# Optimization experiments

Measured on AMD Instinct MI355X. Metric: run time of the kernel, lower is better.

Reference implementation:

```python
import jax, jax.numpy as jnp
import numpy as np

S = 4096            # num tokens (single causal sequence)
HID = 1024          # hidden_size
NH = 16             # num query heads
NKV = 4             # num kv heads
HD = 64             # head_dim
THETA = 10000.0
Q_SIZE = NH * HD
KV_SIZE = NKV * HD


def setup_inputs() -> dict:
    key = jax.random.key(0)
    k1, k2, k3 = jax.random.split(key, 3)
    return {
        "positions": jnp.arange(S, dtype=jnp.int32),
        "hidden_states": jax.random.normal(k1, (S, 2 * HID), dtype=jnp.float32),
        "w_qkv": jax.random.normal(k2, (Q_SIZE + 2 * KV_SIZE, 2 * HID), dtype=jnp.float32) * 0.02,
        "w_o": jax.random.normal(k3, (HID, Q_SIZE), dtype=jnp.float32) * 0.02,
    }


def _rope(x, positions):
    # x: [S, H, HD]; neox-style rotate-half RoPE
    half = HD // 2
    inv_freq = 1.0 / (THETA ** (jnp.arange(0, half, dtype=jnp.float32) / half))
    freqs = positions.astype(jnp.float32)[:, None] * inv_freq  # [S, half]
    cos = jnp.cos(freqs)[:, None, :]  # [S, 1, half]
    sin = jnp.sin(freqs)[:, None, :]
    x1, x2 = x[..., :half], x[..., half:]
    return jnp.concatenate([x1 * cos - x2 * sin, x2 * cos + x1 * sin], axis=-1)


def reference(positions, hidden_states, w_qkv, w_o):
    qkv = hidden_states @ w_qkv.T  # [S, Q_SIZE + 2*KV_SIZE]
    q = qkv[:, :Q_SIZE].reshape(S, NH, HD)
    k = qkv[:, Q_SIZE:Q_SIZE + KV_SIZE].reshape(S, NKV, HD)
    v = qkv[:, Q_SIZE + KV_SIZE:].reshape(S, NKV, HD)
    q = _rope(q, positions)
    k = _rope(k, positions)
    # GQA: group query heads over kv heads
    g = NH // NKV
    qg = q.reshape(S, NKV, g, HD)
    scale = HD ** -0.5
    scores = jnp.einsum("qhgd,thd->hgqt", qg, k) * scale  # [NKV, g, S, S]
    causal = positions[:, None] >= positions[None, :]      # [S, S]
    scores = jnp.where(causal[None, None], scores, jnp.finfo(scores.dtype).min)
    probs = jax.nn.softmax(scores, axis=-1)
    o = jnp.einsum("hgqt,thd->qhgd", probs, v).reshape(S, Q_SIZE)
    return o @ w_o.T  # [S, HID]
```

## Files before the change

### kernel.cpp

```cpp
#include <hip/hip_runtime.h>
#include <math.h>

#define S_LEN   4096
#define NHEADS  16
#define NKVH    4
#define HDIM    64
#define QKV_N   1536
#define HID2    2048
#define OUT_N   1024

typedef __attribute__((ext_vector_type(8))) __bf16 bf16x8;
typedef __attribute__((ext_vector_type(4))) __bf16 bf16x4;
typedef __attribute__((ext_vector_type(4))) float  f32x4;
typedef __attribute__((ext_vector_type(16))) float f32x16;
typedef __attribute__((ext_vector_type(4))) unsigned int u32x4;

#define GL_LDS16(gaddr, laddr)                                                  \
  __builtin_amdgcn_global_load_lds(                                             \
      (const __attribute__((address_space(1))) unsigned int*)(gaddr),           \
      (__attribute__((address_space(3))) unsigned int*)(laddr), 16, 0, 0)

__device__ __forceinline__ unsigned cvt_pk_bf16(float lo, float hi) {
  unsigned r;
  asm("v_cvt_pk_bf16_f32 %0, %1, %2" : "=v"(r) : "v"(lo), "v"(hi));
  return r;
}

__global__ __launch_bounds__(256) void cvt_all(const float* __restrict__ hid,
                                               const float* __restrict__ wq,
                                               const float* __restrict__ wo,
                                               __bf16* __restrict__ hid_bf,
                                               __bf16* __restrict__ wq_bf,
                                               __bf16* __restrict__ wo_bf) {
  const int n1 = S_LEN * HID2;
  const int n2 = QKV_N * HID2;
  int i = (blockIdx.x * blockDim.x + threadIdx.x) * 8;
  const float* src; __bf16* dst; int off;
  if (i < n1)           { src = hid; dst = hid_bf; off = i; }
  else if (i < n1 + n2) { src = wq;  dst = wq_bf;  off = i - n1; }
  else                  { src = wo;  dst = wo_bf;  off = i - n1 - n2; }
  float4 a = *(const float4*)(src + off);
  float4 b = *(const float4*)(src + off + 4);
  bf16x8 o = {(__bf16)a.x,(__bf16)a.y,(__bf16)a.z,(__bf16)a.w,
              (__bf16)b.x,(__bf16)b.y,(__bf16)b.z,(__bf16)b.w};
  *(bf16x8*)(dst + off) = o;
}

__global__ __launch_bounds__(256) void rope_table(const int* __restrict__ positions,
                                                  float* __restrict__ ct,
                                                  float* __restrict__ st) {
  int i = blockIdx.x * blockDim.x + threadIdx.x;
  int s = i >> 5, d = i & 31;
  double inv = pow(10000.0, -(double)d / 32.0);
  double fr = (double)positions[s] * inv;
  ct[i] = (float)cos(fr);
  st[i] = (float)sin(fr);
}

template<int BM, bool C_BF16>
__global__ __launch_bounds__(256) void gemm_db(const __bf16* __restrict__ A,
                                               const __bf16* __restrict__ B,
                                               void* __restrict__ Cp,
                                               int M, int N, int K) {
  constexpr int TM = BM / 32;
  __shared__ __align__(16) __bf16 As[2 * BM * 32];
  __shared__ __align__(16) __bf16 Bs[2 * 128 * 32];
  const int tid  = threadIdx.x;
  const int bm   = blockIdx.x, bn = blockIdx.y;
  const int wave = tid >> 6, lane = tid & 63;
  const int quad = lane >> 4, col = lane & 15;
  const int wm = (wave >> 1) * (BM / 2), wn = (wave & 1) * 64;

  const int lrow = lane >> 2, lcol = (lane & 3) * 8;
  const __bf16* Ag = A + (size_t)(bm * BM + wave * (BM / 4) + lrow) * K + lcol;
  const __bf16* Bg = B + (size_t)(bn * 128 + wave * 32 + lrow) * K + lcol;
  __bf16* AsW = As + wave * (BM / 4) * 32;
  __bf16* BsW = Bs + wave * 32 * 32;

  f32x4 acc[TM][4];
#pragma unroll
  for (int i = 0; i < TM; ++i)
#pragma unroll
    for (int j = 0; j < 4; ++j) acc[i][j] = (f32x4){0.f, 0.f, 0.f, 0.f};

#pragma unroll
  for (int u = 0; u < BM / 64; ++u)
    GL_LDS16(Ag + (size_t)(u * 16) * K, AsW + u * 16 * 32);
  GL_LDS16(Bg,                  BsW);
  GL_LDS16(Bg + (size_t)16 * K, BsW + 16 * 32);
  __syncthreads();

  int cur = 0;
  for (int kk = 0; kk < K; kk += 32) {
    if (kk + 32 < K) {
      const int nxt = cur ^ 1;
#pragma unroll
      for (int u = 0; u < BM / 64; ++u)
        GL_LDS16(Ag + kk + 32 + (size_t)(u * 16) * K,
                 AsW + nxt * BM * 32 + u * 16 * 32);
      GL_LDS16(Bg + kk + 32,                  BsW + nxt * 128 * 32);
      GL_LDS16(Bg + kk + 32 + (size_t)16 * K, BsW + nxt * 128 * 32 + 16 * 32);
    }

    bf16x8 a[TM], b[4];
#pragma unroll
    for (int tm = 0; tm < TM; ++tm)
      a[tm] = *(const bf16x8*)&As[cur * BM * 32 + (wm + tm * 16 + col) * 32 + quad * 8];
#pragma unroll
    for (int tn = 0; tn < 4; ++tn)
      b[tn] = *(const bf16x8*)&Bs[cur * 128 * 32 + (wn + tn * 16 + col) * 32 + quad * 8];
#pragma unroll
    for (int tm = 0; tm < TM; ++tm)
#pragma unroll
      for (int tn = 0; tn < 4; ++tn)
        acc[tm][tn] = __builtin_amdgcn_mfma_f32_16x16x32_bf16(a[tm], b[tn], acc[tm][tn], 0, 0, 0);

    __syncthreads();
    cur ^= 1;
  }

#pragma unroll
  for (int tm = 0; tm < TM; ++tm)
#pragma unroll
    for (int tn = 0; tn < 4; ++tn) {
      int row = bm * BM + wm + tm * 16 + quad * 4;
      int cg  = bn * 128 + wn + tn * 16 + col;
#pragma unroll
      for (int r = 0; r < 4; ++r) {
        if constexpr (C_BF16)
          ((__bf16*)Cp)[(size_t)(row + r) * N + cg] = (__bf16)acc[tm][tn][r];
        else
          ((float*)Cp)[(size_t)(row + r) * N + cg] = acc[tm][tn][r];
      }
    }
}

__global__ __launch_bounds__(256) void rope_cast(const __bf16* __restrict__ qkv,
                                                 const float* __restrict__ ct,
                                                 const float* __restrict__ st,
                                                 __bf16* __restrict__ qb,
                                                 __bf16* __restrict__ kb) {
  int g = blockIdx.x * blockDim.x + threadIdx.x;
  int d = g & 31;
  int rem = g >> 5;
  int head = rem % 20;
  int s = rem / 20;
  bool isq = head < NHEADS;
  const __bf16* src = qkv + (size_t)s * QKV_N + (isq ? head * 64 : 1024 + (head - 16) * 64);
  float c  = ct[s * 32 + d];
  float sn = st[s * 32 + d];
  float x1 = (float)src[d], x2 = (float)src[d + 32];
  float y1 = x1 * c - x2 * sn;
  float y2 = x2 * c + x1 * sn;
  float scl = isq ? 0.18033688011112042f : 1.0f;
  __bf16* dst = isq ? (qb + (size_t)s * 1024 + head * 64)
                    : (kb + (size_t)s * 256 + (head - 16) * 64);
  dst[d]      = (__bf16)(y1 * scl);
  dst[d + 32] = (__bf16)(y2 * scl);
}

__global__ __launch_bounds__(256) void v_transpose(const __bf16* __restrict__ qkv,
                                                   __bf16* __restrict__ vT) {
  __shared__ __align__(16) __bf16 Ts[64][72];
  const int sb = blockIdx.x, kvh = blockIdx.y, t = threadIdx.x;
  const int r = t >> 2, c16 = (t & 3) * 16;
  const __bf16* src = qkv + (size_t)(sb * 64 + r) * QKV_N + 1280 + kvh * 64 + c16;
  bf16x8 v0 = *(const bf16x8*)src;
  bf16x8 v1 = *(const bf16x8*)(src + 8);
#pragma unroll
  for (int u = 0; u < 8; ++u) {
    Ts[c16 + u][r]     = v0[u];
    Ts[c16 + 8 + u][r] = v1[u];
  }
  __syncthreads();
  __bf16* dst = vT + ((size_t)kvh * 64 + r) * S_LEN + sb * 64 + c16;
  *(bf16x8*)dst       = *(const bf16x8*)&Ts[r][c16];
  *(bf16x8*)(dst + 8) = *(const bf16x8*)&Ts[r][c16 + 8];
}

__global__ __launch_bounds__(256, 4) void attn_split(const __bf16* __restrict__ qg,
                                                     const __bf16* __restrict__ kg,
                                                     const __bf16* __restrict__ vg,
                                                     __bf16* __restrict__ op0,
                                                     __bf16* __restrict__ op1,
                                                     float* __restrict__ lp) {
  __shared__ __align__(16) __bf16 lds[18432];
  __bf16* Ks = lds;
  __bf16* Vs = lds + 9216;

  const int tid = threadIdx.x;
  const int h = blockIdx.x;
  const int yy = blockIdx.y;
  const int qq = yy >> 1, split = yy & 1;
  const int qb = (qq < 16) ? qq : 47 - qq;
  const int kvh = h >> 2;
  const int wave = tid >> 6, lane = tid & 63;
  const int r31 = lane & 31, hi = lane >> 5;
  const int hi4 = hi * 4, hi8 = hi * 8;
  const int qbase = qb * 128 + wave * 32;
  const int kt0 = split * (qb + 1);
  const int ktEnd = kt0 + qb + 1;

  {
    const int r = tid >> 1, c = (tid & 1) * 32;
    const __bf16* src = qg + (size_t)(qb * 128 + r) * 1024 + h * 64 + c;
    __bf16* dq = lds + r * 72 + c;
    *(bf16x8*)(dq)      = *(const bf16x8*)(src);
    *(bf16x8*)(dq + 8)  = *(const bf16x8*)(src + 8);
    *(bf16x8*)(dq + 16) = *(const bf16x8*)(src + 16);
    *(bf16x8*)(dq + 24) = *(const bf16x8*)(src + 24);
  }

  const int sr = tid >> 2, sc = (tid & 3) * 16;
  const __bf16* kptr = kg + (size_t)sr * 256 + kvh * 64 + sc;
  const __bf16* vptr = vg + ((size_t)kvh * 64 + sr) * S_LEN + sc;
  bf16x8 kr0 = *(const bf16x8*)(kptr + (size_t)kt0 * 64 * 256);
  bf16x8 kr1 = *(const bf16x8*)(kptr + (size_t)kt0 * 64 * 256 + 8);
  bf16x8 vr0 = *(const bf16x8*)(vptr + (size_t)kt0 * 64);
  bf16x8 vr1 = *(const bf16x8*)(vptr + (size_t)kt0 * 64 + 8);

  __syncthreads();

  bf16x8 qf[4];
#pragma unroll
  for (int dc = 0; dc < 4; ++dc)
    qf[dc] = *(const bf16x8*)&lds[(wave * 32 + r31) * 72 + dc * 16 + hi8];

  __syncthreads();

  f32x16 fz;
#pragma unroll
  for (int g = 0; g < 16; ++g) fz[g] = 0.f;

  f32x16 o[2];
  o[0] = fz; o[1] = fz;
  float lacc = 0.f;

  for (int kt = kt0; kt < ktEnd; ++kt) {
    const int cur = (kt - kt0) & 1;
    {
      __bf16* kd = Ks + cur * 4608 + sr * 72 + sc;
      *(bf16x8*)kd       = kr0;
      *(bf16x8*)(kd + 8) = kr1;
      __bf16* vd = Vs + cur * 4608 + sr * 72 + sc;
      *(bf16x8*)vd       = vr0;
      *(bf16x8*)(vd + 8) = vr1;
    }
    if (kt + 1 < ktEnd) {
      const __bf16* kn = kptr + (size_t)(kt + 1) * 64 * 256;
      const __bf16* vn = vptr + (size_t)(kt + 1) * 64;
      kr0 = *(const bf16x8*)(kn);
      kr1 = *(const bf16x8*)(kn + 8);
      vr0 = *(const bf16x8*)(vn);
      vr1 = *(const bf16x8*)(vn + 8);
    }
    __syncthreads();

    if (kt * 64 > qbase + 31) continue;

    const bool full = (kt * 64 + 63 <= qbase);
    const int thr = qbase + r31 - kt * 64;

    bf16x8 pa[4];
#pragma unroll
    for (int kb = 0; kb < 2; ++kb) {
      bf16x8 kf0 = *(const bf16x8*)&Ks[cur * 4608 + (kb * 32 + r31) * 72 + hi8];
      f32x16 sf = __builtin_amdgcn_mfma_f32_32x32x16_bf16(kf0, qf[0], fz, 0, 0, 0);
#pragma unroll
      for (int dc = 1; dc < 4; ++dc) {
        bf16x8 kf = *(const bf16x8*)&Ks[cur * 4608 + (kb * 32 + r31) * 72 + dc * 16 + hi8];
        sf = __builtin_amdgcn_mfma_f32_32x32x16_bf16(kf, qf[dc], sf, 0, 0, 0);
      }
      float p[16];
#pragma unroll
      for (int g = 0; g < 16; ++g) {
        float e = __builtin_amdgcn_exp2f(sf[g]);
        if (!full) {
          const int krow = kb * 32 + (g & 3) + 8 * (g >> 2) + hi4;
          if (krow > thr) e = 0.f;
        }
        p[g] = e;
      }
#pragma unroll
      for (int m = 0; m < 4; ++m)
        lacc += (p[4 * m] + p[4 * m + 1]) + (p[4 * m + 2] + p[4 * m + 3]);
#pragma unroll
      for (int half = 0; half < 2; ++half) {
        unsigned a0 = cvt_pk_bf16(p[8 * half + 0], p[8 * half + 1]);
        unsigned a1 = cvt_pk_bf16(p[8 * half + 2], p[8 * half + 3]);
        unsigned b0 = cvt_pk_bf16(p[8 * half + 4], p[8 * half + 5]);
        unsigned b1 = cvt_pk_bf16(p[8 * half + 6], p[8 * half + 7]);
        asm("v_permlane32_swap_b32 %0, %1" : "+v"(a0), "+v"(b0));
        asm("v_permlane32_swap_b32 %0, %1" : "+v"(a1), "+v"(b1));
        u32x4 t = {a0, a1, b0, b1};
        pa[kb * 2 + half] = __builtin_bit_cast(bf16x8, t);
      }
    }

#pragma unroll
    for (int dt = 0; dt < 2; ++dt)
#pragma unroll
      for (int kc = 0; kc < 4; ++kc) {
        bf16x8 vf = *(const bf16x8*)&Vs[cur * 4608 + (dt * 32 + r31) * 72 + kc * 16 + hi8];
        o[dt] = __builtin_amdgcn_mfma_f32_32x32x16_bf16(pa[kc], vf, o[dt], 0, 0, 0);
      }
  }

  lacc += __shfl_xor(lacc, 32, 64);
  __syncthreads();
  float* lshw = (float*)lds + wave * 32;
  if (lane < 32) lshw[lane] = lacc;
  asm volatile("s_waitcnt lgkmcnt(0)" ::: "memory");

  __bf16* op = split ? op1 : op0;
#pragma unroll
  for (int g = 0; g < 16; ++g) {
    const int rl = (g & 3) + 8 * (g >> 2) + hi4;
    float l = lshw[rl];
    float linv = (l > 0.f) ? 1.f / l : 0.f;
    const size_t row = (size_t)(qb * 128 + wave * 32 + rl);
    op[row * 1024 + h * 64 + r31]      = (__bf16)(o[0][g] * linv);
    op[row * 1024 + h * 64 + 32 + r31] = (__bf16)(o[1][g] * linv);
  }
  if (lane < 32)
    lp[(size_t)(split * S_LEN + qb * 128 + wave * 32 + lane) * NHEADS + h] = lacc;
}

__global__ __launch_bounds__(256) void attn_combine(const __bf16* __restrict__ op0,
                                                    const __bf16* __restrict__ op1,
                                                    const float* __restrict__ lp,
                                                    __bf16* __restrict__ ob) {
  int i = blockIdx.x * 256 + threadIdx.x;
  int row = i >> 7, c8 = (i & 127) * 8;
  int h = c8 >> 6;
  float l0 = lp[(size_t)row * NHEADS + h];
  float l1 = lp[(size_t)(S_LEN + row) * NHEADS + h];
  float inv = 1.f / (l0 + l1);
  float w0 = l0 * inv, w1 = l1 * inv;
  bf16x8 a = *(const bf16x8*)(op0 + (size_t)row * 1024 + c8);
  bf16x8 b = *(const bf16x8*)(op1 + (size_t)row * 1024 + c8);
  bf16x8 o;
#pragma unroll
  for (int u = 0; u < 8; ++u)
    o[u] = (__bf16)((float)a[u] * w0 + (float)b[u] * w1);
  *(bf16x8*)(ob + (size_t)row * 1024 + c8) = o;
}

extern "C" void kernel_launch(void* const* d_in, const int* in_sizes, int n_in,
                              void* d_out, int out_size, void* d_ws, size_t ws_size,
                              hipStream_t stream) {
  const int*   positions = (const int*)d_in[0];
  const float* hidden    = (const float*)d_in[1];
  const float* w_qkv     = (const float*)d_in[2];
  const float* w_o       = (const float*)d_in[3];
  float* out = (float*)d_out;

  char* ws = (char*)d_ws;
  __bf16* qkv_bf  = (__bf16*)ws;
  __bf16* Opart0  = (__bf16*)ws;
  __bf16* attn_bf = (__bf16*)ws;
  float*  lpart   = (float*)(ws + 8388608);
  __bf16* hid_bf  = (__bf16*)(ws + 12582912);
  __bf16* q_bf    = (__bf16*)(ws + 12582912);
  __bf16* k_bf    = (__bf16*)(ws + 20971520);
  __bf16* vT      = (__bf16*)(ws + 23068672);
  float*  ct      = (float*)(ws + 29360128);
  float*  st      = (float*)(ws + 29884416);
  __bf16* wq_bf   = (__bf16*)(ws + 30408704);
  __bf16* Opart1  = (__bf16*)(ws + 30408704);
  __bf16* wo_bf   = (__bf16*)(ws + 38797312);

  cvt_all<<<(S_LEN * HID2 + QKV_N * HID2 + OUT_N * OUT_N) / 8 / 256, 256, 0, stream>>>(
      hidden, w_qkv, w_o, hid_bf, wq_bf, wo_bf);
  rope_table<<<S_LEN * 32 / 256, 256, 0, stream>>>(positions, ct, st);

  gemm_db<64, true><<<dim3(S_LEN / 64, QKV_N / 128), 256, 0, stream>>>(
      hid_bf, wq_bf, qkv_bf, S_LEN, QKV_N, HID2);

  rope_cast<<<(S_LEN * 20 * 32) / 256, 256, 0, stream>>>(qkv_bf, ct, st, q_bf, k_bf);
  v_transpose<<<dim3(S_LEN / 64, NKVH), 256, 0, stream>>>(qkv_bf, vT);

  attn_split<<<dim3(NHEADS, 64), 256, 0, stream>>>(q_bf, k_bf, vT,
                                                   Opart0, Opart1, lpart);
  attn_combine<<<S_LEN * 128 / 256, 256, 0, stream>>>(Opart0, Opart1, lpart, attn_bf);

  gemm_db<64, false><<<dim3(S_LEN / 64, OUT_N / 128), 256, 0, stream>>>(
      attn_bf, wo_bf, out, S_LEN, OUT_N, OUT_N);
}
```

Before: 221.9 us.

## Balance causal attention work by pairing query blocks and splitting KV four ways

Each attention block now handles a complementary pair of query tiles (pr and 31-pr). Each tile's KV range is split into four partial segments, so every block gets roughly the same number of KV tiles instead of anywhere from 1 to 32. This targets the long-tail imbalance of causal attention. The combine kernel now merges four partial outputs weighted by their row sums. Two of the partial buffers live in the output buffer as scratch. The cost is more partial-output traffic and a heavier combine step, plus reloading Q twice per block.

```diff
diff --git a/kernel.cpp b/kernel.cpp
--- a/kernel.cpp
+++ b/kernel.cpp
@@ -183,6 +183,8 @@
                                                      const __bf16* __restrict__ vg,
                                                      __bf16* __restrict__ op0,
                                                      __bf16* __restrict__ op1,
+                                                     __bf16* __restrict__ op2,
+                                                     __bf16* __restrict__ op3,
                                                      float* __restrict__ lp) {
   __shared__ __align__(16) __bf16 lds[18432];
   __bf16* Ks = lds;
@@ -190,144 +192,156 @@
 
   const int tid = threadIdx.x;
   const int h = blockIdx.x;
-  const int yy = blockIdx.y;
-  const int qq = yy >> 1, split = yy & 1;
-  const int qb = (qq < 16) ? qq : 47 - qq;
+  const int y = blockIdx.y;
+  const int s = y & 1;
+  const int idx = y >> 1;
+  const int fam = idx >> 4;
+  const int pr = idx & 15;
   const int kvh = h >> 2;
   const int wave = tid >> 6, lane = tid & 63;
   const int r31 = lane & 31, hi = lane >> 5;
   const int hi4 = hi * 4, hi8 = hi * 8;
-  const int qbase = qb * 128 + wave * 32;
-  const int kt0 = split * (qb + 1);
-  const int ktEnd = kt0 + qb + 1;
-
-  {
-    const int r = tid >> 1, c = (tid & 1) * 32;
-    const __bf16* src = qg + (size_t)(qb * 128 + r) * 1024 + h * 64 + c;
-    __bf16* dq = lds + r * 72 + c;
-    *(bf16x8*)(dq)      = *(const bf16x8*)(src);
-    *(bf16x8*)(dq + 8)  = *(const bf16x8*)(src + 8);
-    *(bf16x8*)(dq + 16) = *(const bf16x8*)(src + 16);
-    *(bf16x8*)(dq + 24) = *(const bf16x8*)(src + 24);
-  }
-
   const int sr = tid >> 2, sc = (tid & 3) * 16;
   const __bf16* kptr = kg + (size_t)sr * 256 + kvh * 64 + sc;
   const __bf16* vptr = vg + ((size_t)kvh * 64 + sr) * S_LEN + sc;
-  bf16x8 kr0 = *(const bf16x8*)(kptr + (size_t)kt0 * 64 * 256);
-  bf16x8 kr1 = *(const bf16x8*)(kptr + (size_t)kt0 * 64 * 256 + 8);
-  bf16x8 vr0 = *(const bf16x8*)(vptr + (size_t)kt0 * 64);
-  bf16x8 vr1 = *(const bf16x8*)(vptr + (size_t)kt0 * 64 + 8);
-
-  __syncthreads();
-
-  bf16x8 qf[4];
-#pragma unroll
-  for (int dc = 0; dc < 4; ++dc)
-    qf[dc] = *(const bf16x8*)&lds[(wave * 32 + r31) * 72 + dc * 16 + hi8];
-
-  __syncthreads();
 
   f32x16 fz;
 #pragma unroll
   for (int g = 0; g < 16; ++g) fz[g] = 0.f;
 
-  f32x16 o[2];
-  o[0] = fz; o[1] = fz;
-  float lacc = 0.f;
-
-  for (int kt = kt0; kt < ktEnd; ++kt) {
-    const int cur = (kt - kt0) & 1;
+  for (int jp = 0; jp < 2; ++jp) {
+    const int qb = jp ? (31 - pr) : pr;
+    const int m = qb + 1, hh = (m + 1) >> 1;
+    const int ktB = s * m + (fam ? hh : 0);
+    const int ktE = s * m + (fam ? m : hh);
+    const int slot = 2 * s + fam;
+    const int qbase = qb * 128 + wave * 32;
+
+    __syncthreads();
+
     {
-      __bf16* kd = Ks + cur * 4608 + sr * 72 + sc;
-      *(bf16x8*)kd       = kr0;
-      *(bf16x8*)(kd + 8) = kr1;
-      __bf16* vd = Vs + cur * 4608 + sr * 72 + sc;
-      *(bf16x8*)vd       = vr0;
-      *(bf16x8*)(vd + 8) = vr1;
+      const int r = tid >> 1, c = (tid & 1) * 32;
+      const __bf16* src = qg + (size_t)(qb * 128 + r) * 1024 + h * 64 + c;
+      __bf16* dq = lds + r * 72 + c;
+      *(bf16x8*)(dq)      = *(const bf16x8*)(src);
+      *(bf16x8*)(dq + 8)  = *(const bf16x8*)(src + 8);
+      *(bf16x8*)(dq + 16) = *(const bf16x8*)(src + 16);
+      *(bf16x8*)(dq + 24) = *(const bf16x8*)(src + 24);
     }
-    if (kt + 1 < ktEnd) {
-      const __bf16* kn = kptr + (size_t)(kt + 1) * 64 * 256;
-      const __bf16* vn = vptr + (size_t)(kt + 1) * 64;
-      kr0 = *(const bf16x8*)(kn);
-      kr1 = *(const bf16x8*)(kn + 8);
-      vr0 = *(const bf16x8*)(vn);
-      vr1 = *(const bf16x8*)(vn + 8);
+
+    bf16x8 kr0 = *(const bf16x8*)(kptr + (size_t)ktB * 64 * 256);
+    bf16x8 kr1 = *(const bf16x8*)(kptr + (size_t)ktB * 64 * 256 + 8);
+    bf16x8 vr0 = *(const bf16x8*)(vptr + (size_t)ktB * 64);
+    bf16x8 vr1 = *(const bf16x8*)(vptr + (size_t)ktB * 64 + 8);
+
+    __syncthreads();
+
+    bf16x8 qf[4];
+#pragma unroll
+    for (int dc = 0; dc < 4; ++dc)
+      qf[dc] = *(const bf16x8*)&lds[(wave * 32 + r31) * 72 + dc * 16 + hi8];
+
+    __syncthreads();
+
+    f32x16 o[2];
+    o[0] = fz; o[1] = fz;
+    float lacc = 0.f;
+
+    for (int kt = ktB; kt < ktE; ++kt) {
+      const int cur = (kt - ktB) & 1;
+      {
+        __bf16* kd = Ks + cur * 4608 + sr * 72 + sc;
+        *(bf16x8*)kd       = kr0;
+        *(bf16x8*)(kd + 8) = kr1;
+        __bf16* vd = Vs + cur * 4608 + sr * 72 + sc;
+        *(bf16x8*)vd       = vr0;
+        *(bf16x8*)(vd + 8) = vr1;
+      }
+      if (kt + 1 < ktE) {
+        const __bf16* kn = kptr + (size_t)(kt + 1) * 64 * 256;
+        const __bf16* vn = vptr + (size_t)(kt + 1) * 64;
+        kr0 = *(const bf16x8*)(kn);
+        kr1 = *(const bf16x8*)(kn + 8);
+        vr0 = *(const bf16x8*)(vn);
+        vr1 = *(const bf16x8*)(vn + 8);
+      }
+      __syncthreads();
+
+      if (kt * 64 > qbase + 31) continue;
+
+      const bool full = (kt * 64 + 63 <= qbase);
+      const int thr = qbase + r31 - kt * 64;
+
+      bf16x8 pa[4];
+#pragma unroll
+      for (int kb = 0; kb < 2; ++kb) {
+        bf16x8 kf0 = *(const bf16x8*)&Ks[cur * 4608 + (kb * 32 + r31) * 72 + hi8];
+        f32x16 sf = __builtin_amdgcn_mfma_f32_32x32x16_bf16(kf0, qf[0], fz, 0, 0, 0);
+#pragma unroll
+        for (int dc = 1; dc < 4; ++dc) {
+          bf16x8 kf = *(const bf16x8*)&Ks[cur * 4608 + (kb * 32 + r31) * 72 + dc * 16 + hi8];
+          sf = __builtin_amdgcn_mfma_f32_32x32x16_bf16(kf, qf[dc], sf, 0, 0, 0);
+        }
+        float p[16];
+#pragma unroll
+        for (int g = 0; g < 16; ++g) {
+          float e = __builtin_amdgcn_exp2f(sf[g]);
+          if (!full) {
+            const int krow = kb * 32 + (g & 3) + 8 * (g >> 2) + hi4;
+            if (krow > thr) e = 0.f;
+          }
+          p[g] = e;
+        }
+#pragma unroll
+        for (int mm = 0; mm < 4; ++mm)
+          lacc += (p[4 * mm] + p[4 * mm + 1]) + (p[4 * mm + 2] + p[4 * mm + 3]);
+#pragma unroll
+        for (int half = 0; half < 2; ++half) {
+          unsigned a0 = cvt_pk_bf16(p[8 * half + 0], p[8 * half + 1]);
+          unsigned a1 = cvt_pk_bf16(p[8 * half + 2], p[8 * half + 3]);
+          unsigned b0 = cvt_pk_bf16(p[8 * half + 4], p[8 * half + 5]);
+          unsigned b1 = cvt_pk_bf16(p[8 * half + 6], p[8 * half + 7]);
+          asm("v_permlane32_swap_b32 %0, %1" : "+v"(a0), "+v"(b0));
+          asm("v_permlane32_swap_b32 %0, %1" : "+v"(a1), "+v"(b1));
+          u32x4 t = {a0, a1, b0, b1};
+          pa[kb * 2 + half] = __builtin_bit_cast(bf16x8, t);
+        }
+      }
+
+#pragma unroll
+      for (int dt = 0; dt < 2; ++dt)
+#pragma unroll
+        for (int kc = 0; kc < 4; ++kc) {
+          bf16x8 vf = *(const bf16x8*)&Vs[cur * 4608 + (dt * 32 + r31) * 72 + kc * 16 + hi8];
+          o[dt] = __builtin_amdgcn_mfma_f32_32x32x16_bf16(pa[kc], vf, o[dt], 0, 0, 0);
+        }
     }
+
+    lacc += __shfl_xor(lacc, 32, 64);
     __syncthreads();
-
-    if (kt * 64 > qbase + 31) continue;
-
-    const bool full = (kt * 64 + 63 <= qbase);
-    const int thr = qbase + r31 - kt * 64;
-
-    bf16x8 pa[4];
-#pragma unroll
-    for (int kb = 0; kb < 2; ++kb) {
-      bf16x8 kf0 = *(const bf16x8*)&Ks[cur * 4608 + (kb * 32 + r31) * 72 + hi8];
-      f32x16 sf = __builtin_amdgcn_mfma_f32_32x32x16_bf16(kf0, qf[0], fz, 0, 0, 0);
-#pragma unroll
-      for (int dc = 1; dc < 4; ++dc) {
-        bf16x8 kf = *(const bf16x8*)&Ks[cur * 4608 + (kb * 32 + r31) * 72 + dc * 16 + hi8];
-        sf = __builtin_amdgcn_mfma_f32_32x32x16_bf16(kf, qf[dc], sf, 0, 0, 0);
-      }
-      float p[16];
-#pragma unroll
-      for (int g = 0; g < 16; ++g) {
-        float e = __builtin_amdgcn_exp2f(sf[g]);
-        if (!full) {
-          const int krow = kb * 32 + (g & 3) + 8 * (g >> 2) + hi4;
-          if (krow > thr) e = 0.f;
-        }
-        p[g] = e;
-      }
-#pragma unroll
-      for (int m = 0; m < 4; ++m)
-        lacc += (p[4 * m] + p[4 * m + 1]) + (p[4 * m + 2] + p[4 * m + 3]);
-#pragma unroll
-      for (int half = 0; half < 2; ++half) {
-        unsigned a0 = cvt_pk_bf16(p[8 * half + 0], p[8 * half + 1]);
-        unsigned a1 = cvt_pk_bf16(p[8 * half + 2], p[8 * half + 3]);
-        unsigned b0 = cvt_pk_bf16(p[8 * half + 4], p[8 * half + 5]);
-        unsigned b1 = cvt_pk_bf16(p[8 * half + 6], p[8 * half + 7]);
-        asm("v_permlane32_swap_b32 %0, %1" : "+v"(a0), "+v"(b0));
-        asm("v_permlane32_swap_b32 %0, %1" : "+v"(a1), "+v"(b1));
-        u32x4 t = {a0, a1, b0, b1};
-        pa[kb * 2 + half] = __builtin_bit_cast(bf16x8, t);
-      }
+    float* lshw = (float*)lds + wave * 32;
+    if (lane < 32) lshw[lane] = lacc;
+    asm volatile("s_waitcnt lgkmcnt(0)" ::: "memory");
+
+    __bf16* op = (slot == 0) ? op0 : (slot == 1) ? op1 : (slot == 2) ? op2 : op3;
+#pragma unroll
+    for (int g = 0; g < 16; ++g) {
+      const int rl = (g & 3) + 8 * (g >> 2) + hi4;
+      float l = lshw[rl];
+      float linv = (l > 0.f) ? 1.f / l : 0.f;
+      const size_t row = (size_t)(qb * 128 + wave * 32 + rl);
+      op[row * 1024 + h * 64 + r31]      = (__bf16)(o[0][g] * linv);
+      op[row * 1024 + h * 64 + 32 + r31] = (__bf16)(o[1][g] * linv);
     }
-
-#pragma unroll
-    for (int dt = 0; dt < 2; ++dt)
-#pragma unroll
-      for (int kc = 0; kc < 4; ++kc) {
-        bf16x8 vf = *(const bf16x8*)&Vs[cur * 4608 + (dt * 32 + r31) * 72 + kc * 16 + hi8];
-        o[dt] = __builtin_amdgcn_mfma_f32_32x32x16_bf16(pa[kc], vf, o[dt], 0, 0, 0);
-      }
-  }
-
-  lacc += __shfl_xor(lacc, 32, 64);
-  __syncthreads();
-  float* lshw = (float*)lds + wave * 32;
-  if (lane < 32) lshw[lane] = lacc;
-  asm volatile("s_waitcnt lgkmcnt(0)" ::: "memory");
-
-  __bf16* op = split ? op1 : op0;
-#pragma unroll
-  for (int g = 0; g < 16; ++g) {
-    const int rl = (g & 3) + 8 * (g >> 2) + hi4;
-    float l = lshw[rl];
-    float linv = (l > 0.f) ? 1.f / l : 0.f;
-    const size_t row = (size_t)(qb * 128 + wave * 32 + rl);
-    op[row * 1024 + h * 64 + r31]      = (__bf16)(o[0][g] * linv);
-    op[row * 1024 + h * 64 + 32 + r31] = (__bf16)(o[1][g] * linv);
-  }
-  if (lane < 32)
-    lp[(size_t)(split * S_LEN + qb * 128 + wave * 32 + lane) * NHEADS + h] = lacc;
+    if (lane < 32)
+      lp[(size_t)(slot * S_LEN + qb * 128 + wave * 32 + lane) * NHEADS + h] = lacc;
+  }
 }
 
 __global__ __launch_bounds__(256) void attn_combine(const __bf16* __restrict__ op0,
                                                     const __bf16* __restrict__ op1,
+                                                    const __bf16* __restrict__ op2,
+                                                    const __bf16* __restrict__ op3,
                                                     const float* __restrict__ lp,
                                                     __bf16* __restrict__ ob) {
   int i = blockIdx.x * 256 + threadIdx.x;
@@ -335,14 +349,35 @@
   int h = c8 >> 6;
   float l0 = lp[(size_t)row * NHEADS + h];
   float l1 = lp[(size_t)(S_LEN + row) * NHEADS + h];
-  float inv = 1.f / (l0 + l1);
-  float w0 = l0 * inv, w1 = l1 * inv;
-  bf16x8 a = *(const bf16x8*)(op0 + (size_t)row * 1024 + c8);
-  bf16x8 b = *(const bf16x8*)(op1 + (size_t)row * 1024 + c8);
+  float l2 = lp[(size_t)(2 * S_LEN + row) * NHEADS + h];
+  float l3 = lp[(size_t)(3 * S_LEN + row) * NHEADS + h];
+  float inv = 1.f / (l0 + l1 + l2 + l3);
+  float acc[8];
+#pragma unroll
+  for (int u = 0; u < 8; ++u) acc[u] = 0.f;
+  {
+    bf16x8 a = *(const bf16x8*)(op0 + (size_t)row * 1024 + c8);
+#pragma unroll
+    for (int u = 0; u < 8; ++u) acc[u] += (l0 > 0.f) ? (float)a[u] * l0 : 0.f;
+  }
+  {
+    bf16x8 a = *(const bf16x8*)(op1 + (size_t)row * 1024 + c8);
+#pragma unroll
+    for (int u = 0; u < 8; ++u) acc[u] += (l1 > 0.f) ? (float)a[u] * l1 : 0.f;
+  }
+  {
+    bf16x8 a = *(const bf16x8*)(op2 + (size_t)row * 1024 + c8);
+#pragma unroll
+    for (int u = 0; u < 8; ++u) acc[u] += (l2 > 0.f) ? (float)a[u] * l2 : 0.f;
+  }
+  {
+    bf16x8 a = *(const bf16x8*)(op3 + (size_t)row * 1024 + c8);
+#pragma unroll
+    for (int u = 0; u < 8; ++u) acc[u] += (l3 > 0.f) ? (float)a[u] * l3 : 0.f;
+  }
   bf16x8 o;
 #pragma unroll
-  for (int u = 0; u < 8; ++u)
-    o[u] = (__bf16)((float)a[u] * w0 + (float)b[u] * w1);
+  for (int u = 0; u < 8; ++u) o[u] = (__bf16)(acc[u] * inv);
   *(bf16x8*)(ob + (size_t)row * 1024 + c8) = o;
 }
 
@@ -369,6 +404,8 @@
   __bf16* wq_bf   = (__bf16*)(ws + 30408704);
   __bf16* Opart1  = (__bf16*)(ws + 30408704);
   __bf16* wo_bf   = (__bf16*)(ws + 38797312);
+  __bf16* Opart2  = (__bf16*)d_out;
+  __bf16* Opart3  = (__bf16*)((char*)d_out + 8388608);
 
   cvt_all<<<(S_LEN * HID2 + QKV_N * HID2 + OUT_N * OUT_N) / 8 / 256, 256, 0, stream>>>(
       hidden, w_qkv, w_o, hid_bf, wq_bf, wo_bf);
@@ -381,8 +418,10 @@
   v_transpose<<<dim3(S_LEN / 64, NKVH), 256, 0, stream>>>(qkv_bf, vT);
 
   attn_split<<<dim3(NHEADS, 64), 256, 0, stream>>>(q_bf, k_bf, vT,
-                                                   Opart0, Opart1, lpart);
-  attn_combine<<<S_LEN * 128 / 256, 256, 0, stream>>>(Opart0, Opart1, lpart, attn_bf);
+                                                   Opart0, Opart1, Opart2, Opart3,
+                                                   lpart);
+  attn_combine<<<S_LEN * 128 / 256, 256, 0, stream>>>(Opart0, Opart1, Opart2, Opart3,
+                                                      lpart, attn_bf);
 
   gemm_db<64, false><<<dim3(S_LEN / 64, OUT_N / 128), 256, 0, stream>>>(
       attn_bf, wo_bf, out, S_LEN, OUT_N, OUT_N);
```

New measurement: 237.7 us. 7.1% more time.

## Fuse RoPE and Q scaling into the QKV GEMM epilogue

Applied to the files above, without the earlier changes.

The QKV projection GEMM now applies rotary embedding and the query scale directly in its epilogue for the Q and K column blocks. It writes rotated bf16 Q and K straight into the output buffer, which serves as scratch until the final projection runs. V blocks are still stored as before. This removes the separate rope_cast kernel, along with its extra read of the QKV intermediate and its launch. In exchange the GEMM epilogue does extra cos/sin table loads and branching for Q/K tiles.

```diff
diff --git a/kernel.cpp b/kernel.cpp
--- a/kernel.cpp
+++ b/kernel.cpp
@@ -8,6 +8,7 @@
 #define QKV_N   1536
 #define HID2    2048
 #define OUT_N   1024
+#define QSCALE  0.18033688011112042f
 
 typedef __attribute__((ext_vector_type(8))) __bf16 bf16x8;
 typedef __attribute__((ext_vector_type(4))) __bf16 bf16x4;
@@ -57,10 +58,14 @@
   st[i] = (float)sin(fr);
 }
 
-template<int BM, bool C_BF16>
+template<int BM, int EPI>
 __global__ __launch_bounds__(256) void gemm_db(const __bf16* __restrict__ A,
                                                const __bf16* __restrict__ B,
                                                void* __restrict__ Cp,
+                                               const float* __restrict__ ct,
+                                               const float* __restrict__ st,
+                                               __bf16* __restrict__ qd,
+                                               __bf16* __restrict__ kd,
                                                int M, int N, int K) {
   constexpr int TM = BM / 32;
   __shared__ __align__(16) __bf16 As[2 * BM * 32];
@@ -119,44 +124,54 @@
     cur ^= 1;
   }
 
-#pragma unroll
-  for (int tm = 0; tm < TM; ++tm)
-#pragma unroll
-    for (int tn = 0; tn < 4; ++tn) {
-      int row = bm * BM + wm + tm * 16 + quad * 4;
-      int cg  = bn * 128 + wn + tn * 16 + col;
-#pragma unroll
-      for (int r = 0; r < 4; ++r) {
-        if constexpr (C_BF16)
-          ((__bf16*)Cp)[(size_t)(row + r) * N + cg] = (__bf16)acc[tm][tn][r];
-        else
+  if constexpr (EPI == 2) {
+    if (bn < 10) {
+      const float scl = (bn < 8) ? QSCALE : 1.0f;
+      __bf16* dst    = (bn < 8) ? qd : kd;
+      const int strd = (bn < 8) ? 1024 : 256;
+      const int base = (bn < 8) ? 0 : 1024;
+#pragma unroll
+      for (int tm = 0; tm < TM; ++tm)
+#pragma unroll
+        for (int tn = 0; tn < 2; ++tn) {
+          const int row0 = bm * BM + wm + tm * 16 + quad * 4;
+          const int cg   = bn * 128 + wn + tn * 16 + col;
+          const int dcol = cg - base;
+          const int d    = tn * 16 + col;
+#pragma unroll
+          for (int r = 0; r < 4; ++r) {
+            const int srow = row0 + r;
+            float c  = ct[srow * 32 + d];
+            float sn = st[srow * 32 + d];
+            float x1 = acc[tm][tn][r], x2 = acc[tm][tn + 2][r];
+            dst[(size_t)srow * strd + dcol]      = (__bf16)((x1 * c - x2 * sn) * scl);
+            dst[(size_t)srow * strd + dcol + 32] = (__bf16)((x2 * c + x1 * sn) * scl);
+          }
+        }
+    } else {
+#pragma unroll
+      for (int tm = 0; tm < TM; ++tm)
+#pragma unroll
+        for (int tn = 0; tn < 4; ++tn) {
+          int row = bm * BM + wm + tm * 16 + quad * 4;
+          int cg  = bn * 128 + wn + tn * 16 + col;
+#pragma unroll
+          for (int r = 0; r < 4; ++r)
+            ((__bf16*)Cp)[(size_t)(row + r) * N + cg] = (__bf16)acc[tm][tn][r];
+        }
+    }
+  } else {
+#pragma unroll
+    for (int tm = 0; tm < TM; ++tm)
+#pragma unroll
+      for (int tn = 0; tn < 4; ++tn) {
+        int row = bm * BM + wm + tm * 16 + quad * 4;
+        int cg  = bn * 128 + wn + tn * 16 + col;
+#pragma unroll
+        for (int r = 0; r < 4; ++r)
           ((float*)Cp)[(size_t)(row + r) * N + cg] = acc[tm][tn][r];
       }
-    }
-}
-
-__global__ __launch_bounds__(256) void rope_cast(const __bf16* __restrict__ qkv,
-                                                 const float* __restrict__ ct,
-                                                 const float* __restrict__ st,
-                                                 __bf16* __restrict__ qb,
-                                                 __bf16* __restrict__ kb) {
-  int g = blockIdx.x * blockDim.x + threadIdx.x;
-  int d = g & 31;
-  int rem = g >> 5;
-  int head = rem % 20;
-  int s = rem / 20;
-  bool isq = head < NHEADS;
-  const __bf16* src = qkv + (size_t)s * QKV_N + (isq ? head * 64 : 1024 + (head - 16) * 64);
-  float c  = ct[s * 32 + d];
-  float sn = st[s * 32 + d];
-  float x1 = (float)src[d], x2 = (float)src[d + 32];
-  float y1 = x1 * c - x2 * sn;
-  float y2 = x2 * c + x1 * sn;
-  float scl = isq ? 0.18033688011112042f : 1.0f;
-  __bf16* dst = isq ? (qb + (size_t)s * 1024 + head * 64)
-                    : (kb + (size_t)s * 256 + (head - 16) * 64);
-  dst[d]      = (__bf16)(y1 * scl);
-  dst[d + 32] = (__bf16)(y2 * scl);
+  }
 }
 
 __global__ __launch_bounds__(256) void v_transpose(const __bf16* __restrict__ qkv,
@@ -361,29 +376,28 @@
   __bf16* attn_bf = (__bf16*)ws;
   float*  lpart   = (float*)(ws + 8388608);
   __bf16* hid_bf  = (__bf16*)(ws + 12582912);
-  __bf16* q_bf    = (__bf16*)(ws + 12582912);
-  __bf16* k_bf    = (__bf16*)(ws + 20971520);
   __bf16* vT      = (__bf16*)(ws + 23068672);
   float*  ct      = (float*)(ws + 29360128);
   float*  st      = (float*)(ws + 29884416);
   __bf16* wq_bf   = (__bf16*)(ws + 30408704);
   __bf16* Opart1  = (__bf16*)(ws + 30408704);
   __bf16* wo_bf   = (__bf16*)(ws + 38797312);
+  __bf16* q_bf    = (__bf16*)d_out;
+  __bf16* k_bf    = (__bf16*)((char*)d_out + 8388608);
 
   cvt_all<<<(S_LEN * HID2 + QKV_N * HID2 + OUT_N * OUT_N) / 8 / 256, 256, 0, stream>>>(
       hidden, w_qkv, w_o, hid_bf, wq_bf, wo_bf);
   rope_table<<<S_LEN * 32 / 256, 256, 0, stream>>>(positions, ct, st);
 
-  gemm_db<64, true><<<dim3(S_LEN / 64, QKV_N / 128), 256, 0, stream>>>(
-      hid_bf, wq_bf, qkv_bf, S_LEN, QKV_N, HID2);
-
-  rope_cast<<<(S_LEN * 20 * 32) / 256, 256, 0, stream>>>(qkv_bf, ct, st, q_bf, k_bf);
+  gemm_db<64, 2><<<dim3(S_LEN / 64, QKV_N / 128), 256, 0, stream>>>(
+      hid_bf, wq_bf, qkv_bf, ct, st, q_bf, k_bf, S_LEN, QKV_N, HID2);
+
   v_transpose<<<dim3(S_LEN / 64, NKVH), 256, 0, stream>>>(qkv_bf, vT);
 
   attn_split<<<dim3(NHEADS, 64), 256, 0, stream>>>(q_bf, k_bf, vT,
                                                    Opart0, Opart1, lpart);
   attn_combine<<<S_LEN * 128 / 256, 256, 0, stream>>>(Opart0, Opart1, lpart, attn_bf);
 
-  gemm_db<64, false><<<dim3(S_LEN / 64, OUT_N / 128), 256, 0, stream>>>(
-      attn_bf, wo_bf, out, S_LEN, OUT_N, OUT_N);
-}
+  gemm_db<64, 0><<<dim3(S_LEN / 64, OUT_N / 128), 256, 0, stream>>>(
+      attn_bf, wo_bf, out, nullptr, nullptr, nullptr, nullptr, S_LEN, OUT_N, OUT_N);
+}
```

After: 221.8 us. Within noise of the previous version (-0.1%).
